# Kernel tuning notes

Measured on AMD Instinct MI355X. Metric: run time of the kernel, lower is better.

The kernel has to match this reference:

```python
import jax, jax.numpy as jnp
import numpy as np

NEG_SLOPE = 0.01  # torch.nn.LeakyReLU default


def setup_inputs() -> dict:
    key = jax.random.key(0)
    ks = jax.random.split(key, 9)
    B, S, F1, F2, N, M, E, L = 2, 256, 512, 512, 20000, 2, 320000, 3
    x = jax.random.normal(ks[0], (B, S, F1), dtype=jnp.float32)
    nodes = jax.random.normal(ks[1], (N, M, F2), dtype=jnp.float32)
    edge_index = jax.random.randint(ks[2], (2, E), 0, N, dtype=jnp.int32)
    Wp = jax.random.normal(ks[3], (F1, F2), dtype=jnp.float32) * 0.02  # torch Linear weight [out,in]
    bp = jax.random.normal(ks[4], (F1,), dtype=jnp.float32) * 0.02
    gcn_W = jax.random.normal(ks[5], (L, S, S), dtype=jnp.float32) * 0.05  # stored as [in,out]
    gcn_b = jax.random.normal(ks[6], (L, S), dtype=jnp.float32) * 0.02
    w_bp = jax.random.normal(ks[7], (S,), dtype=jnp.float32) * 0.05
    b_bp = jax.random.normal(ks[8], (1,), dtype=jnp.float32) * 0.02
    return {"x": x, "nodes": nodes, "edge_index": edge_index, "Wp": Wp, "bp": bp,
            "gcn_W": gcn_W, "gcn_b": gcn_b, "w_bp": w_bp, "b_bp": b_bp}


def reference(x, nodes, edge_index, Wp, bp, gcn_W, gcn_b, w_bp, b_bp):
    # Eval mode: dropout layers are identity.
    N = nodes.shape[0]
    L = gcn_W.shape[0]
    proj = nodes @ Wp.T + bp                         # [N, M, F1]
    score = jnp.einsum('bsk,nmk->bsn', x, proj)      # sum over M and F1 -> [B, S, N]
    h = score.transpose(0, 2, 1)                     # beliefs [B, N, S]

    # GCN normalization with self-loops: D^{-1/2} (A + I) D^{-1/2}
    src, dst = edge_index[0], edge_index[1]
    loop = jnp.arange(N, dtype=edge_index.dtype)
    row = jnp.concatenate([src, loop])               # message sources
    col = jnp.concatenate([dst, loop])               # message targets
    deg = jnp.zeros((N,), dtype=h.dtype).at[col].add(1.0)
    dinv = deg ** -0.5                               # deg >= 1 due to self-loops
    norm = dinv[row] * dinv[col]                     # [E+N]

    for l in range(L):
        hw = h @ gcn_W[l]                            # [B, N, S]
        msg = hw[:, row, :] * norm[None, :, None]    # gather + scale
        agg = jnp.zeros_like(hw).at[:, col, :].add(msg) + gcn_b[l]
        h = jax.nn.leaky_relu(agg, NEG_SLOPE)

    # belief_projection: Linear(S, 1) then squeeze -> [B, N]
    return h @ w_bp + b_bp[0]
```

## Files before the change

### kernel.cpp

```cpp
#include <hip/hip_runtime.h>
#include <cstddef>
#include <cstdint>

#define NN 20000

typedef short frag16 __attribute__((ext_vector_type(8)));
typedef float f32x4 __attribute__((ext_vector_type(4)));

__device__ inline unsigned short f32_to_bf16(float f) {
    uint32_t u = __float_as_uint(f);
    u += 0x7FFFu + ((u >> 16) & 1u);
    return (unsigned short)(u >> 16);
}

__device__ inline float4 dec4(uint2 v) {
    float4 r;
    r.x = __uint_as_float(v.x << 16);
    r.y = __uint_as_float(v.x & 0xffff0000u);
    r.z = __uint_as_float(v.y << 16);
    r.w = __uint_as_float(v.y & 0xffff0000u);
    return r;
}

__device__ inline void dec8_add(uint4 v, float* a) {
    a[0] += __uint_as_float(v.x << 16);
    a[1] += __uint_as_float(v.x & 0xffff0000u);
    a[2] += __uint_as_float(v.y << 16);
    a[3] += __uint_as_float(v.y & 0xffff0000u);
    a[4] += __uint_as_float(v.z << 16);
    a[5] += __uint_as_float(v.z & 0xffff0000u);
    a[6] += __uint_as_float(v.w << 16);
    a[7] += __uint_as_float(v.w & 0xffff0000u);
}

__global__ __launch_bounds__(256) void prep(
    const float* __restrict__ nodes, const float* __restrict__ x,
    const float* __restrict__ gcn_W, const float* __restrict__ bp,
    const int* __restrict__ src, const int* __restrict__ dst,
    unsigned short* __restrict__ nsum16, unsigned short* __restrict__ WT,
    float* __restrict__ Tf, float* __restrict__ cvec,
    int* __restrict__ cnt, int* __restrict__ csr, int E)
{
    __shared__ __align__(16) char shmem[8704];
    const int blk = blockIdx.x, tid = threadIdx.x;

    if (blk < 64) {
        float* As = (float*)shmem;
        float* Bs = As + 1024;
        int t = blk;
        int b = t >> 5, rem = t & 31;
        int s0 = (rem >> 3) * 64, f0 = (rem & 7) * 64;
        const float* W1 = gcn_W;
        const float* xb = x + (size_t)b * 256 * 512;
        int kk = tid >> 4, c4 = (tid & 15) << 2;
        int tm = tid >> 4, tn = tid & 15;
        float acc[4][4] = {};
        float4 av = *(const float4*)(W1 + (size_t)kk * 256 + s0 + c4);
        float4 bv = *(const float4*)(xb + (size_t)kk * 512 + f0 + c4);
        for (int k0 = 0; k0 < 256; k0 += 16) {
            __syncthreads();
            *(float4*)&As[kk * 64 + c4] = av;
            *(float4*)&Bs[kk * 64 + c4] = bv;
            __syncthreads();
            if (k0 + 16 < 256) {
                av = *(const float4*)(W1 + (size_t)(k0 + 16 + kk) * 256 + s0 + c4);
                bv = *(const float4*)(xb + (size_t)(k0 + 16 + kk) * 512 + f0 + c4);
            }
            #pragma unroll
            for (int k = 0; k < 16; ++k) {
                float a[4], bb[4];
                *(float4*)a  = *(const float4*)&As[k * 64 + (tm << 2)];
                *(float4*)bb = *(const float4*)&Bs[k * 64 + (tn << 2)];
                #pragma unroll
                for (int i = 0; i < 4; ++i)
                    #pragma unroll
                    for (int j = 0; j < 4; ++j) acc[i][j] += a[i] * bb[j];
            }
        }
        #pragma unroll
        for (int i = 0; i < 4; ++i) {
            int row = b * 256 + s0 + (tm << 2) + i;
            *(float4*)(Tf + (size_t)row * 512 + f0 + (tn << 2)) =
                make_float4(acc[i][0], acc[i][1], acc[i][2], acc[i][3]);
        }
    } else if (blk < 96) {
        unsigned short (*tsh)[68] = (unsigned short(*)[68])shmem;
        int t = blk - 64;
        int l = t >> 4, rem = t & 15;
        int c0 = (rem & 3) * 64, r0 = (rem >> 2) * 64;
        const float* inp = gcn_W + (size_t)(l + 1) * 65536;
        unsigned short* outp = WT + (size_t)l * 65536;
        int tx = tid & 15, ty = tid >> 4;
        #pragma unroll
        for (int rr = 0; rr < 4; ++rr) {
            int r = ty * 4 + rr;
            float4 v = *(const float4*)(inp + (size_t)(r0 + r) * 256 + c0 + tx * 4);
            tsh[tx * 4 + 0][r] = f32_to_bf16(v.x);
            tsh[tx * 4 + 1][r] = f32_to_bf16(v.y);
            tsh[tx * 4 + 2][r] = f32_to_bf16(v.z);
            tsh[tx * 4 + 3][r] = f32_to_bf16(v.w);
        }
        __syncthreads();
        #pragma unroll
        for (int cc = 0; cc < 4; ++cc) {
            int c = ty * 4 + cc;
            ushort4 o = *(ushort4*)&tsh[c][tx * 4];
            *(ushort4*)(outp + (size_t)(c0 + c) * 256 + r0 + tx * 4) = o;
        }
    } else if (blk < 224) {
        int row = (blk - 96) * 4 + (tid >> 6);
        int lane = tid & 63;
        const float* xr = x + (size_t)row * 512;
        float s = 0.f;
        #pragma unroll
        for (int k = 0; k < 512; k += 64) s += xr[k + lane] * bp[k + lane];
        #pragma unroll
        for (int off = 32; off; off >>= 1) s += __shfl_down(s, off);
        if (lane == 0) cvec[row] = 2.0f * s;
    } else if (blk < 224 + 2512) {
        int g = (blk - 224) * 256 + tid;
        int n = g >> 5, c = (g & 31) << 4;
        uint4 o0, o1;
        if (n < NN) {
            const float* r0 = nodes + (size_t)n * 1024 + c;
            const float* r1 = r0 + 512;
            float4 a0 = *(const float4*)(r0 + 0),  a1 = *(const float4*)(r0 + 4);
            float4 a2 = *(const float4*)(r0 + 8),  a3 = *(const float4*)(r0 + 12);
            float4 b0 = *(const float4*)(r1 + 0),  b1 = *(const float4*)(r1 + 4);
            float4 b2 = *(const float4*)(r1 + 8),  b3 = *(const float4*)(r1 + 12);
            o0.x = ((uint32_t)f32_to_bf16(a0.y + b0.y) << 16) | f32_to_bf16(a0.x + b0.x);
            o0.y = ((uint32_t)f32_to_bf16(a0.w + b0.w) << 16) | f32_to_bf16(a0.z + b0.z);
            o0.z = ((uint32_t)f32_to_bf16(a1.y + b1.y) << 16) | f32_to_bf16(a1.x + b1.x);
            o0.w = ((uint32_t)f32_to_bf16(a1.w + b1.w) << 16) | f32_to_bf16(a1.z + b1.z);
            o1.x = ((uint32_t)f32_to_bf16(a2.y + b2.y) << 16) | f32_to_bf16(a2.x + b2.x);
            o1.y = ((uint32_t)f32_to_bf16(a2.w + b2.w) << 16) | f32_to_bf16(a2.z + b2.z);
            o1.z = ((uint32_t)f32_to_bf16(a3.y + b3.y) << 16) | f32_to_bf16(a3.x + b3.x);
            o1.w = ((uint32_t)f32_to_bf16(a3.w + b3.w) << 16) | f32_to_bf16(a3.z + b3.z);
        } else {
            o0 = make_uint4(0, 0, 0, 0); o1 = o0;
        }
        *(uint4*)(nsum16 + (size_t)n * 512 + c) = o0;
        *(uint4*)(nsum16 + (size_t)n * 512 + c + 8) = o1;
    } else {
        int e = (blk - 2736) * 256 + tid;
        if (e < E) {
            int d = dst[e];
            int pos = atomicAdd(&cnt[d], 1);
            if (pos < 64) csr[(d << 6) + pos] = src[e];
        }
    }
}

__global__ __launch_bounds__(256) void mid(
    const float* __restrict__ Tf, const float* __restrict__ Wp,
    const float* __restrict__ gcn_W, const float* __restrict__ cvec,
    unsigned short* __restrict__ Ub, float* __restrict__ cb2)
{
    const int blk = blockIdx.x, tid = threadIdx.x;
    if (blk >= 64) {
        int idx = (blk - 64) * 256 + tid;
        int b = idx >> 8, s = idx & 255;
        float sum = 0.f;
        for (int sp = 0; sp < 256; ++sp)
            sum += gcn_W[(size_t)sp * 256 + s] * cvec[b * 256 + sp];
        cb2[idx] = sum;
        return;
    }
    __shared__ float As[16][68];
    __shared__ float Bs[16][64];
    int bm = (blk >> 3) * 64, bn = (blk & 7) * 64;
    int arow = tid >> 2, acol = (tid & 3) << 2;
    int brow = tid >> 4, bcol = (tid & 15) << 2;
    int tm = tid >> 4, tn = tid & 15;
    float acc[4][4] = {};
    float4 av = *(const float4*)(Tf + (size_t)(bm + arow) * 512 + acol);
    float4 bv = *(const float4*)(Wp + (size_t)brow * 512 + bn + bcol);
    for (int k0 = 0; k0 < 512; k0 += 16) {
        __syncthreads();
        As[acol + 0][arow] = av.x; As[acol + 1][arow] = av.y;
        As[acol + 2][arow] = av.z; As[acol + 3][arow] = av.w;
        *(float4*)&Bs[brow][bcol] = bv;
        __syncthreads();
        if (k0 + 16 < 512) {
            av = *(const float4*)(Tf + (size_t)(bm + arow) * 512 + k0 + 16 + acol);
            bv = *(const float4*)(Wp + (size_t)(k0 + 16 + brow) * 512 + bn + bcol);
        }
        #pragma unroll
        for (int k = 0; k < 16; ++k) {
            float a[4], b[4];
            *(float4*)a = *(const float4*)&As[k][tm << 2];
            *(float4*)b = *(const float4*)&Bs[k][tn << 2];
            #pragma unroll
            for (int i = 0; i < 4; ++i)
                #pragma unroll
                for (int j = 0; j < 4; ++j) acc[i][j] += a[i] * b[j];
        }
    }
    #pragma unroll
    for (int i = 0; i < 4; ++i) {
        int row = bm + (tm << 2) + i;
        ushort4 o;
        o.x = f32_to_bf16(acc[i][0]); o.y = f32_to_bf16(acc[i][1]);
        o.z = f32_to_bf16(acc[i][2]); o.w = f32_to_bf16(acc[i][3]);
        *(ushort4*)(Ub + (size_t)row * 512 + bn + (tn << 2)) = o;
    }
}

__global__ __launch_bounds__(256) void mgemm(
    const unsigned short* __restrict__ A, const unsigned short* __restrict__ BT,
    int K, int N, int mode,
    const float* __restrict__ cb2, const int* __restrict__ cnt,
    unsigned short* __restrict__ C)
{
    __shared__ __align__(16) unsigned short As[128 * 32];
    __shared__ __align__(16) unsigned short Bs[128 * 32];
    const int bm = blockIdx.y * 128, bn = blockIdx.x * 128;
    const int tid = threadIdx.x;
    const int lane = tid & 63, w = tid >> 6;
    const int wm = (w >> 1) << 6, wn = (w & 1) << 6;
    const int r = lane & 15, q = lane >> 4;

    f32x4 acc[4][4] = {};

    for (int k0 = 0; k0 < K; k0 += 32) {
        __syncthreads();
        #pragma unroll
        for (int t = 0; t < 2; ++t) {
            int c = t * 256 + w * 64 + lane;
            int row = c >> 2, col = (c & 3) << 3;
            __builtin_amdgcn_global_load_lds(
                (const __attribute__((address_space(1))) void*)(A + (size_t)(bm + row) * K + k0 + col),
                (__attribute__((address_space(3))) void*)(As + (size_t)(t * 256 + w * 64) * 8),
                16, 0, 0);
            __builtin_amdgcn_global_load_lds(
                (const __attribute__((address_space(1))) void*)(BT + (size_t)(bn + row) * K + k0 + col),
                (__attribute__((address_space(3))) void*)(Bs + (size_t)(t * 256 + w * 64) * 8),
                16, 0, 0);
        }
        __syncthreads();
        frag16 af[4], bf[4];
        #pragma unroll
        for (int i = 0; i < 4; ++i)
            af[i] = *(const frag16*)(As + ((wm + i * 16 + r) << 5) + (q << 3));
        #pragma unroll
        for (int j = 0; j < 4; ++j)
            bf[j] = *(const frag16*)(Bs + ((wn + j * 16 + r) << 5) + (q << 3));
        #pragma unroll
        for (int i = 0; i < 4; ++i)
            #pragma unroll
            for (int j = 0; j < 4; ++j)
                acc[i][j] = __builtin_amdgcn_mfma_f32_16x16x32_bf16(af[i], bf[j], acc[i][j], 0, 0, 0);
    }

    #pragma unroll
    for (int i = 0; i < 4; ++i) {
        #pragma unroll
        for (int rg = 0; rg < 4; ++rg) {
            int m = bm + wm + i * 16 + (q << 2) + rg;
            float sc;
            int b2 = 0, node = m;
            if (mode == 1) {
                int nc = m > NN - 1 ? NN - 1 : m;
                sc = rsqrtf((float)cnt[nc] + 1.0f);
            } else {
                b2 = m >= NN;
                node = m - b2 * NN;
                int nc = node > NN - 1 ? NN - 1 : node;
                sc = rsqrtf((float)cnt[nc] + 1.0f);
                if (node > 20095) node = 20095;
            }
            #pragma unroll
            for (int j = 0; j < 4; ++j) {
                int n = bn + wn + j * 16 + r;
                if (mode == 1) {
                    float v = (acc[i][j][rg] + cb2[n]) * sc;
                    C[(size_t)m * 512 + n] = f32_to_bf16(v);
                } else {
                    float v = acc[i][j][rg] * sc;
                    C[(size_t)node * 512 + (b2 << 8) + n] = f32_to_bf16(v);
                }
            }
        }
    }
}

__global__ __launch_bounds__(256) void aggregate_s(
    const unsigned short* __restrict__ hw, const int* __restrict__ cnt,
    const int* __restrict__ csr, const float* __restrict__ bias,
    unsigned short* __restrict__ hout,
    const float* __restrict__ w_bp, const float* __restrict__ b_bp,
    float* __restrict__ out)
{
    int n = blockIdx.x * 4 + (threadIdx.x >> 6);
    int lane = threadIdx.x & 63;
    const unsigned short* rowp = hw + (lane << 3);

    int deg = cnt[n]; if (deg > 64) deg = 64;
    int myidx = csr[(n << 6) + lane];

    float acc[8] = {};
    dec8_add(*(const uint4*)(rowp + (size_t)n * 512), acc);
    int e = 0;
    for (; e + 8 <= deg; e += 8) {
        int s0 = __shfl(myidx, e + 0), s1 = __shfl(myidx, e + 1);
        int s2 = __shfl(myidx, e + 2), s3 = __shfl(myidx, e + 3);
        int s4 = __shfl(myidx, e + 4), s5 = __shfl(myidx, e + 5);
        int s6 = __shfl(myidx, e + 6), s7 = __shfl(myidx, e + 7);
        uint4 u0 = *(const uint4*)(rowp + (size_t)s0 * 512);
        uint4 u1 = *(const uint4*)(rowp + (size_t)s1 * 512);
        uint4 u2 = *(const uint4*)(rowp + (size_t)s2 * 512);
        uint4 u3 = *(const uint4*)(rowp + (size_t)s3 * 512);
        uint4 u4 = *(const uint4*)(rowp + (size_t)s4 * 512);
        uint4 u5 = *(const uint4*)(rowp + (size_t)s5 * 512);
        uint4 u6 = *(const uint4*)(rowp + (size_t)s6 * 512);
        uint4 u7 = *(const uint4*)(rowp + (size_t)s7 * 512);
        dec8_add(u0, acc); dec8_add(u1, acc); dec8_add(u2, acc); dec8_add(u3, acc);
        dec8_add(u4, acc); dec8_add(u5, acc); dec8_add(u6, acc); dec8_add(u7, acc);
    }
    if (e + 4 <= deg) {
        int s0 = __shfl(myidx, e + 0), s1 = __shfl(myidx, e + 1);
        int s2 = __shfl(myidx, e + 2), s3 = __shfl(myidx, e + 3);
        uint4 u0 = *(const uint4*)(rowp + (size_t)s0 * 512);
        uint4 u1 = *(const uint4*)(rowp + (size_t)s1 * 512);
        uint4 u2 = *(const uint4*)(rowp + (size_t)s2 * 512);
        uint4 u3 = *(const uint4*)(rowp + (size_t)s3 * 512);
        dec8_add(u0, acc); dec8_add(u1, acc); dec8_add(u2, acc); dec8_add(u3, acc);
        e += 4;
    }
    for (; e < deg; ++e) {
        int s0 = __shfl(myidx, e);
        dec8_add(*(const uint4*)(rowp + (size_t)s0 * 512), acc);
    }

    float dn = rsqrtf((float)deg + 1.0f);
    int b = lane >> 5;
    int sc = (lane & 31) << 3;
    float bl[8];
    *(float4*)&bl[0] = *(const float4*)(bias + sc);
    *(float4*)&bl[4] = *(const float4*)(bias + sc + 4);
    float v[8];
    #pragma unroll
    for (int j = 0; j < 8; ++j) {
        v[j] = fmaf(dn, acc[j], bl[j]);
        v[j] = v[j] > 0.f ? v[j] : 0.01f * v[j];
    }

    if (out) {
        float w[8];
        *(float4*)&w[0] = *(const float4*)(w_bp + sc);
        *(float4*)&w[4] = *(const float4*)(w_bp + sc + 4);
        float sum = 0.f;
        #pragma unroll
        for (int j = 0; j < 8; ++j) sum += v[j] * w[j];
        #pragma unroll
        for (int off = 16; off; off >>= 1) sum += __shfl_xor(sum, off);
        if ((lane & 31) == 0) out[b * NN + n] = sum + b_bp[0];
    } else {
        uint4 o;
        o.x = ((uint32_t)f32_to_bf16(v[1]) << 16) | f32_to_bf16(v[0]);
        o.y = ((uint32_t)f32_to_bf16(v[3]) << 16) | f32_to_bf16(v[2]);
        o.z = ((uint32_t)f32_to_bf16(v[5]) << 16) | f32_to_bf16(v[4]);
        o.w = ((uint32_t)f32_to_bf16(v[7]) << 16) | f32_to_bf16(v[6]);
        *(uint4*)(hout + ((size_t)(b * NN + n)) * 256 + sc) = o;
    }
}

extern "C" void kernel_launch(void* const* d_in, const int* in_sizes, int n_in,
                              void* d_out, int out_size, void* d_ws, size_t ws_size,
                              hipStream_t stream) {
    const float* x     = (const float*)d_in[0];
    const float* nodes = (const float*)d_in[1];
    const int*   eidx  = (const int*)d_in[2];
    const float* Wp    = (const float*)d_in[3];
    const float* bp    = (const float*)d_in[4];
    const float* gcn_W = (const float*)d_in[5];
    const float* gcn_b = (const float*)d_in[6];
    const float* w_bp  = (const float*)d_in[7];
    const float* b_bp  = (const float*)d_in[8];
    const int E = in_sizes[2] / 2;

    char* w = (char*)d_ws;
    auto alloc = [&](size_t bytes) { char* p = w; w += (bytes + 255) & ~(size_t)255; return p; };
    unsigned short* nsum16 = (unsigned short*)alloc((size_t)20096 * 512 * 2);
    unsigned short* hw16   = (unsigned short*)alloc((size_t)20096 * 512 * 2);
    unsigned short* hA     = (unsigned short*)alloc((size_t)40192 * 256 * 2);
    unsigned short* hB     = (unsigned short*)alloc((size_t)40192 * 256 * 2);
    float* Tf  = (float*)alloc((size_t)512 * 512 * 4);
    unsigned short* Ub = (unsigned short*)alloc((size_t)512 * 512 * 2);
    unsigned short* WT = (unsigned short*)alloc((size_t)2 * 256 * 256 * 2);
    float* cvec = (float*)alloc(512 * 4);
    float* cb2  = (float*)alloc(512 * 4);
    int*   cnt  = (int*)alloc((size_t)NN * 4);
    int*   csr  = (int*)alloc((size_t)NN * 64 * 4);

    hipMemsetAsync(cnt, 0, (size_t)NN * 4, stream);

    const int cntBlks = (E + 255) / 256;
    prep<<<cntBlks + 64 + 2512 + 32 + 128, 256, 0, stream>>>(
        nodes, x, gcn_W, bp, eidx, eidx + E, nsum16, WT, Tf, cvec, cnt, csr, E);
    mid<<<66, 256, 0, stream>>>(Tf, Wp, gcn_W, cvec, Ub, cb2);

    mgemm<<<dim3(4, 157), 256, 0, stream>>>(nsum16, Ub, 512, 512, 1, cb2, cnt, hw16);

    aggregate_s<<<5000, 256, 0, stream>>>(hw16, cnt, csr, gcn_b + 0, hA,
                                          w_bp, b_bp, nullptr);
    mgemm<<<dim3(2, 313), 256, 0, stream>>>(hA, WT, 256, 256, 2, nullptr, cnt, hw16);
    aggregate_s<<<5000, 256, 0, stream>>>(hw16, cnt, csr, gcn_b + 256, hB,
                                          w_bp, b_bp, nullptr);
    mgemm<<<dim3(2, 313), 256, 0, stream>>>(hB, WT + 65536, 256, 256, 2, nullptr, cnt, hw16);
    aggregate_s<<<5000, 256, 0, stream>>>(hw16, cnt, csr, gcn_b + 512, nullptr,
                                          w_bp, b_bp, (float*)d_out);
}
```

Measured before the change: 378.2 us.

## Split aggregation columns across 8 blocks per node group with 8-lane subgroups

The GCN aggregation kernel changes from one 64-lane wavefront per node to 8-lane groups per node, with each block handling one of 8 column slices for 32 nodes. Each block now gathers only 128 bytes per neighbour row, which gives many more independent node gathers in flight and better latency hiding for the irregular degree. The final layer writes per-slice partial dot products to a buffer, and a small extra kernel sums them and adds the bias. This costs one more launch and reloads the CSR indices once per slice.

After: 368.3 us. 1.03x faster.

```diff
diff --git a/kernel.cpp b/kernel.cpp
--- a/kernel.cpp
+++ b/kernel.cpp
@@ -11,15 +11,6 @@
     uint32_t u = __float_as_uint(f);
     u += 0x7FFFu + ((u >> 16) & 1u);
     return (unsigned short)(u >> 16);
-}
-
-__device__ inline float4 dec4(uint2 v) {
-    float4 r;
-    r.x = __uint_as_float(v.x << 16);
-    r.y = __uint_as_float(v.x & 0xffff0000u);
-    r.z = __uint_as_float(v.y << 16);
-    r.w = __uint_as_float(v.y & 0xffff0000u);
-    return r;
 }
 
 __device__ inline void dec8_add(uint4 v, float* a) {
@@ -284,84 +275,97 @@
     }
 }
 
-__global__ __launch_bounds__(256) void aggregate_s(
+__global__ __launch_bounds__(256) void aggregate_x(
     const unsigned short* __restrict__ hw, const int* __restrict__ cnt,
     const int* __restrict__ csr, const float* __restrict__ bias,
     unsigned short* __restrict__ hout,
-    const float* __restrict__ w_bp, const float* __restrict__ b_bp,
-    float* __restrict__ out)
+    const float* __restrict__ w_bp, float* __restrict__ pout)
 {
-    int n = blockIdx.x * 4 + (threadIdx.x >> 6);
-    int lane = threadIdx.x & 63;
-    const unsigned short* rowp = hw + (lane << 3);
+    const int s  = blockIdx.x & 7;
+    const int nb = blockIdx.x >> 3;
+    const int tid = threadIdx.x;
+    const int g = tid >> 3;
+    const int j = tid & 7;
+    const int n = nb * 32 + g;
+    const int lb = (tid & 63) & 56;
+
+    const unsigned short* rowp = hw + (s << 6) + (j << 3);
 
     int deg = cnt[n]; if (deg > 64) deg = 64;
-    int myidx = csr[(n << 6) + lane];
 
     float acc[8] = {};
     dec8_add(*(const uint4*)(rowp + (size_t)n * 512), acc);
-    int e = 0;
-    for (; e + 8 <= deg; e += 8) {
-        int s0 = __shfl(myidx, e + 0), s1 = __shfl(myidx, e + 1);
-        int s2 = __shfl(myidx, e + 2), s3 = __shfl(myidx, e + 3);
-        int s4 = __shfl(myidx, e + 4), s5 = __shfl(myidx, e + 5);
-        int s6 = __shfl(myidx, e + 6), s7 = __shfl(myidx, e + 7);
-        uint4 u0 = *(const uint4*)(rowp + (size_t)s0 * 512);
-        uint4 u1 = *(const uint4*)(rowp + (size_t)s1 * 512);
-        uint4 u2 = *(const uint4*)(rowp + (size_t)s2 * 512);
-        uint4 u3 = *(const uint4*)(rowp + (size_t)s3 * 512);
-        uint4 u4 = *(const uint4*)(rowp + (size_t)s4 * 512);
-        uint4 u5 = *(const uint4*)(rowp + (size_t)s5 * 512);
-        uint4 u6 = *(const uint4*)(rowp + (size_t)s6 * 512);
-        uint4 u7 = *(const uint4*)(rowp + (size_t)s7 * 512);
-        dec8_add(u0, acc); dec8_add(u1, acc); dec8_add(u2, acc); dec8_add(u3, acc);
-        dec8_add(u4, acc); dec8_add(u5, acc); dec8_add(u6, acc); dec8_add(u7, acc);
-    }
-    if (e + 4 <= deg) {
-        int s0 = __shfl(myidx, e + 0), s1 = __shfl(myidx, e + 1);
-        int s2 = __shfl(myidx, e + 2), s3 = __shfl(myidx, e + 3);
-        uint4 u0 = *(const uint4*)(rowp + (size_t)s0 * 512);
-        uint4 u1 = *(const uint4*)(rowp + (size_t)s1 * 512);
-        uint4 u2 = *(const uint4*)(rowp + (size_t)s2 * 512);
-        uint4 u3 = *(const uint4*)(rowp + (size_t)s3 * 512);
-        dec8_add(u0, acc); dec8_add(u1, acc); dec8_add(u2, acc); dec8_add(u3, acc);
-        e += 4;
-    }
-    for (; e < deg; ++e) {
-        int s0 = __shfl(myidx, e);
-        dec8_add(*(const uint4*)(rowp + (size_t)s0 * 512), acc);
+
+    for (int e0 = 0; e0 < deg; e0 += 8) {
+        int idx = csr[(n << 6) + e0 + j];
+        int m = deg - e0;
+        if (m >= 8) {
+            int s0 = __shfl(idx, lb + 0), s1 = __shfl(idx, lb + 1);
+            int s2 = __shfl(idx, lb + 2), s3 = __shfl(idx, lb + 3);
+            int s4 = __shfl(idx, lb + 4), s5 = __shfl(idx, lb + 5);
+            int s6 = __shfl(idx, lb + 6), s7 = __shfl(idx, lb + 7);
+            uint4 u0 = *(const uint4*)(rowp + (size_t)s0 * 512);
+            uint4 u1 = *(const uint4*)(rowp + (size_t)s1 * 512);
+            uint4 u2 = *(const uint4*)(rowp + (size_t)s2 * 512);
+            uint4 u3 = *(const uint4*)(rowp + (size_t)s3 * 512);
+            uint4 u4 = *(const uint4*)(rowp + (size_t)s4 * 512);
+            uint4 u5 = *(const uint4*)(rowp + (size_t)s5 * 512);
+            uint4 u6 = *(const uint4*)(rowp + (size_t)s6 * 512);
+            uint4 u7 = *(const uint4*)(rowp + (size_t)s7 * 512);
+            dec8_add(u0, acc); dec8_add(u1, acc); dec8_add(u2, acc); dec8_add(u3, acc);
+            dec8_add(u4, acc); dec8_add(u5, acc); dec8_add(u6, acc); dec8_add(u7, acc);
+        } else {
+            for (int t = 0; t < m; ++t) {
+                int se = __shfl(idx, lb + t);
+                dec8_add(*(const uint4*)(rowp + (size_t)se * 512), acc);
+            }
+        }
     }
 
     float dn = rsqrtf((float)deg + 1.0f);
-    int b = lane >> 5;
-    int sc = (lane & 31) << 3;
+    int colb = ((s & 3) << 6) + (j << 3);
     float bl[8];
-    *(float4*)&bl[0] = *(const float4*)(bias + sc);
-    *(float4*)&bl[4] = *(const float4*)(bias + sc + 4);
+    *(float4*)&bl[0] = *(const float4*)(bias + colb);
+    *(float4*)&bl[4] = *(const float4*)(bias + colb + 4);
     float v[8];
     #pragma unroll
-    for (int j = 0; j < 8; ++j) {
-        v[j] = fmaf(dn, acc[j], bl[j]);
-        v[j] = v[j] > 0.f ? v[j] : 0.01f * v[j];
-    }
-
-    if (out) {
-        float w[8];
-        *(float4*)&w[0] = *(const float4*)(w_bp + sc);
-        *(float4*)&w[4] = *(const float4*)(w_bp + sc + 4);
-        float sum = 0.f;
-        #pragma unroll
-        for (int j = 0; j < 8; ++j) sum += v[j] * w[j];
-        #pragma unroll
-        for (int off = 16; off; off >>= 1) sum += __shfl_xor(sum, off);
-        if ((lane & 31) == 0) out[b * NN + n] = sum + b_bp[0];
-    } else {
+    for (int t = 0; t < 8; ++t) {
+        v[t] = fmaf(dn, acc[t], bl[t]);
+        v[t] = v[t] > 0.f ? v[t] : 0.01f * v[t];
+    }
+
+    if (hout) {
+        int b = s >> 2;
         uint4 o;
         o.x = ((uint32_t)f32_to_bf16(v[1]) << 16) | f32_to_bf16(v[0]);
         o.y = ((uint32_t)f32_to_bf16(v[3]) << 16) | f32_to_bf16(v[2]);
         o.z = ((uint32_t)f32_to_bf16(v[5]) << 16) | f32_to_bf16(v[4]);
         o.w = ((uint32_t)f32_to_bf16(v[7]) << 16) | f32_to_bf16(v[6]);
-        *(uint4*)(hout + ((size_t)(b * NN + n)) * 256 + sc) = o;
+        *(uint4*)(hout + ((size_t)(b * NN + n)) * 256 + colb) = o;
+    } else {
+        float w4[8];
+        *(float4*)&w4[0] = *(const float4*)(w_bp + colb);
+        *(float4*)&w4[4] = *(const float4*)(w_bp + colb + 4);
+        float sum = 0.f;
+        #pragma unroll
+        for (int t = 0; t < 8; ++t) sum += v[t] * w4[t];
+        sum += __shfl_xor(sum, 1);
+        sum += __shfl_xor(sum, 2);
+        sum += __shfl_xor(sum, 4);
+        if (j == 0) pout[s * NN + n] = sum;
+    }
+}
+
+__global__ __launch_bounds__(256) void finishk(
+    const float* __restrict__ pout, const float* __restrict__ b_bp,
+    float* __restrict__ out)
+{
+    int i = blockIdx.x * 256 + threadIdx.x;
+    if (i < 2 * NN) {
+        int b = i >= NN;
+        int n = i - b * NN;
+        const float* p = pout + b * 4 * NN + n;
+        out[i] = b_bp[0] + p[0] + p[NN] + p[2 * NN] + p[3 * NN];
     }
 }
 
@@ -390,6 +394,7 @@
     unsigned short* WT = (unsigned short*)alloc((size_t)2 * 256 * 256 * 2);
     float* cvec = (float*)alloc(512 * 4);
     float* cb2  = (float*)alloc(512 * 4);
+    float* pout = (float*)alloc((size_t)8 * NN * 4);
     int*   cnt  = (int*)alloc((size_t)NN * 4);
     int*   csr  = (int*)alloc((size_t)NN * 64 * 4);
 
@@ -402,12 +407,10 @@
 
     mgemm<<<dim3(4, 157), 256, 0, stream>>>(nsum16, Ub, 512, 512, 1, cb2, cnt, hw16);
 
-    aggregate_s<<<5000, 256, 0, stream>>>(hw16, cnt, csr, gcn_b + 0, hA,
-                                          w_bp, b_bp, nullptr);
+    aggregate_x<<<5000, 256, 0, stream>>>(hw16, cnt, csr, gcn_b + 0, hA, w_bp, pout);
     mgemm<<<dim3(2, 313), 256, 0, stream>>>(hA, WT, 256, 256, 2, nullptr, cnt, hw16);
-    aggregate_s<<<5000, 256, 0, stream>>>(hw16, cnt, csr, gcn_b + 256, hB,
-                                          w_bp, b_bp, nullptr);
+    aggregate_x<<<5000, 256, 0, stream>>>(hw16, cnt, csr, gcn_b + 256, hB, w_bp, pout);
     mgemm<<<dim3(2, 313), 256, 0, stream>>>(hB, WT + 65536, 256, 256, 2, nullptr, cnt, hw16);
-    aggregate_s<<<5000, 256, 0, stream>>>(hw16, cnt, csr, gcn_b + 512, nullptr,
-                                          w_bp, b_bp, (float*)d_out);
-}
+    aggregate_x<<<5000, 256, 0, stream>>>(hw16, cnt, csr, gcn_b + 512, nullptr, w_bp, pout);
+    finishk<<<157, 256, 0, stream>>>(pout, b_bp, (float*)d_out);
+}
```
